# Kernel optimization log

Measured on AMD Instinct MI355X. Metric: run time of the kernel, lower is better.

## Reference

```python
import jax, jax.numpy as jnp
import numpy as np


def setup_inputs() -> dict:
    key = jax.random.key(0)
    kq, kk, kv = jax.random.split(key, 3)
    B, H, S, D = 2, 16, 2048, 64
    return {
        "query": jax.random.normal(kq, (B, H, S, D), dtype=jnp.float32),
        "key": jax.random.normal(kk, (B, H, S, D), dtype=jnp.float32),
        "value": jax.random.normal(kv, (B, H, S, D), dtype=jnp.float32),
    }


def reference(query, key, value):
    # scores = Q K^T / sqrt(d_k)   -> [B, H, S, S]
    d_k = query.shape[-1]
    scale = 1.0 / jnp.sqrt(jnp.asarray(d_k, dtype=query.dtype))
    scores = jnp.einsum("bhqd,bhkd->bhqk", query, key) * scale
    # mask=None path (the module's mask path is unreachable due to a source bug)
    p_attn = jax.nn.softmax(scores, axis=-1)
    out = jnp.einsum("bhqk,bhkd->bhqd", p_attn, value)
    return (out, p_attn)
```

## Files before the change

kernel.cpp:

```cpp
#include <hip/hip_runtime.h>
#include <hip/hip_bf16.h>
#include <cstdint>
#include <cstddef>

#define S_LEN 2048
#define D_HEAD 64
#define NBH 32
#define NELEM 4194304
#define SUP 128

typedef __attribute__((ext_vector_type(8))) short short8;
typedef __attribute__((ext_vector_type(4))) float f32x4;

__device__ __forceinline__ short f2bf(float f) {
    union { float f; uint32_t u; } v; v.f = f;
    uint32_t u = v.u + 0x7FFFu + ((v.u >> 16) & 1u);
    return (short)(u >> 16);
}

__device__ __forceinline__ uint32_t pkbf(float lo, float hi) {
    return ((uint32_t)(uint16_t)f2bf(hi) << 16) | (uint32_t)(uint16_t)f2bf(lo);
}

__global__ void convert_kf_kernel(const float* __restrict__ K, short* __restrict__ Kf) {
    const int s = blockIdx.x * 256 + threadIdx.x;
    const int l = s & 63;
    const int p = (s >> 6) & 1;
    const int g = (s >> 7) & 127;
    const int bh = s >> 14;
    const float* src = K + ((size_t)bh * S_LEN + g * 16 + (l & 15)) * D_HEAD
                         + p * 32 + (l >> 4) * 8;
    short8 y;
    #pragma unroll
    for (int e = 0; e < 8; ++e) y[e] = f2bf(src[e]);
    *reinterpret_cast<short8*>(Kf + (size_t)s * 8) = y;
}

__global__ void transpose_vf_kernel(const float* __restrict__ V, short* __restrict__ Vf) {
    __shared__ float tile[64][65];
    const int bh = blockIdx.y;
    const int s0 = blockIdx.x * 64;
    const int d = threadIdx.x & 63;
    const int r = threadIdx.x >> 6;
    const float* vp = V + ((size_t)bh * S_LEN + s0) * D_HEAD;
    #pragma unroll
    for (int i = 0; i < 16; ++i) {
        int srow = i * 4 + r;
        tile[srow][d] = vp[(size_t)srow * D_HEAD + d];
    }
    __syncthreads();
    #pragma unroll
    for (int h = 0; h < 2; ++h) {
        const int sl = h * 256 + threadIdx.x;
        const int ti = sl >> 8;
        const int vt = (sl >> 6) & 3;
        const int l  = sl & 63;
        const int lrow = l & 15, lgrp = l >> 4;
        short8 y;
        #pragma unroll
        for (int e = 0; e < 8; ++e)
            y[e] = f2bf(tile[ti * 32 + lgrp * 8 + e][vt * 16 + lrow]);
        *reinterpret_cast<short8*>(
            Vf + ((((size_t)bh * 64 + (s0 >> 5) + ti) * 4 + vt) * 64 + l) * 8) = y;
    }
}

__launch_bounds__(256, 2)
__global__ void attn_kernel(const float* __restrict__ Q,
                            const short* __restrict__ Kf,
                            const short* __restrict__ Vf,
                            float* __restrict__ Out,
                            float* __restrict__ P) {
    __shared__ __align__(16) float stage[4][2][16][SUP];

    const int lane = threadIdx.x & 63;
    const int w    = threadIdx.x >> 6;
    const int b    = blockIdx.y * 16 + blockIdx.x;
    const int swzb = (b & 7) * 64 + (b >> 3);
    const int bx   = swzb & 15;
    const int bh   = swzb >> 4;
    const int qb   = bx * 128 + w * 32;
    const int lrow = lane & 15;
    const int lgrp = lane >> 4;
    const float scale = 0.125f;

    short8 qa0A, qa1A, qa0B, qa1B;
    {
        const float* qrA = Q + ((size_t)bh * S_LEN + qb + lrow) * D_HEAD + lgrp * 8;
        const float* qrB = qrA + 16 * D_HEAD;
        #pragma unroll
        for (int e = 0; e < 8; ++e) qa0A[e] = f2bf(qrA[e]);
        #pragma unroll
        for (int e = 0; e < 8; ++e) qa1A[e] = f2bf(qrA[e + 32]);
        #pragma unroll
        for (int e = 0; e < 8; ++e) qa0B[e] = f2bf(qrB[e]);
        #pragma unroll
        for (int e = 0; e < 8; ++e) qa1B[e] = f2bf(qrB[e + 32]);
    }

    const short* Kp = Kf + (size_t)bh * (S_LEN * D_HEAD);
    const short* Vp = Vf + (size_t)bh * (S_LEN * D_HEAD);
    const int lofs = lane * 8;

    const int srcA = ((lane & 15) + ((lane >> 4) & 1) * 32) << 2;
    const int srcB = srcA + (16 << 2);
    const bool glow = (lgrp < 2);

    float lA = 0.f, lB = 0.f;
    f32x4 accA[4] = {}, accB[4] = {};
    for (int j0 = 0; j0 < S_LEN; j0 += 32) {
        const short* kg = Kp + (size_t)(j0 >> 4) * 1024;
        short8 k00 = *reinterpret_cast<const short8*>(kg + lofs);
        short8 k01 = *reinterpret_cast<const short8*>(kg + 512 + lofs);
        short8 k10 = *reinterpret_cast<const short8*>(kg + 1024 + lofs);
        short8 k11 = *reinterpret_cast<const short8*>(kg + 1536 + lofs);
        const short* vg = Vp + (size_t)(j0 >> 5) * 2048;
        short8 bv0 = *reinterpret_cast<const short8*>(vg + lofs);
        short8 bv1 = *reinterpret_cast<const short8*>(vg + 512 + lofs);
        short8 bv2 = *reinterpret_cast<const short8*>(vg + 1024 + lofs);
        short8 bv3 = *reinterpret_cast<const short8*>(vg + 1536 + lofs);

        {
            f32x4 c0 = {0.f, 0.f, 0.f, 0.f};
            f32x4 c1 = {0.f, 0.f, 0.f, 0.f};
            c0 = __builtin_amdgcn_mfma_f32_16x16x32_bf16(k00, qa0A, c0, 0, 0, 0);
            c0 = __builtin_amdgcn_mfma_f32_16x16x32_bf16(k01, qa1A, c0, 0, 0, 0);
            c1 = __builtin_amdgcn_mfma_f32_16x16x32_bf16(k10, qa0A, c1, 0, 0, 0);
            c1 = __builtin_amdgcn_mfma_f32_16x16x32_bf16(k11, qa1A, c1, 0, 0, 0);
            float e0[4], e1[4];
            #pragma unroll
            for (int rr = 0; rr < 4; ++rr) {
                e0[rr] = __expf(c0[rr] * scale);
                e1[rr] = __expf(c1[rr] * scale);
                lA += e0[rr] + e1[rr];
            }
            int w00 = (int)pkbf(e0[0], e0[1]);
            int w01 = (int)pkbf(e0[2], e0[3]);
            int w10 = (int)pkbf(e1[0], e1[1]);
            int w11 = (int)pkbf(e1[2], e1[3]);
            int t0 = __builtin_amdgcn_ds_bpermute(srcA, w00);
            int t1 = __builtin_amdgcn_ds_bpermute(srcA, w01);
            int t2 = __builtin_amdgcn_ds_bpermute(srcB, w00);
            int t3 = __builtin_amdgcn_ds_bpermute(srcB, w01);
            int u0 = __builtin_amdgcn_ds_bpermute(srcA, w10);
            int u1 = __builtin_amdgcn_ds_bpermute(srcA, w11);
            int u2 = __builtin_amdgcn_ds_bpermute(srcB, w10);
            int u3 = __builtin_amdgcn_ds_bpermute(srcB, w11);
            union { short8 s8; int wd[4]; } fr;
            fr.wd[0] = glow ? t0 : u0;
            fr.wd[1] = glow ? t1 : u1;
            fr.wd[2] = glow ? t2 : u2;
            fr.wd[3] = glow ? t3 : u3;
            accA[0] = __builtin_amdgcn_mfma_f32_16x16x32_bf16(fr.s8, bv0, accA[0], 0, 0, 0);
            accA[1] = __builtin_amdgcn_mfma_f32_16x16x32_bf16(fr.s8, bv1, accA[1], 0, 0, 0);
            accA[2] = __builtin_amdgcn_mfma_f32_16x16x32_bf16(fr.s8, bv2, accA[2], 0, 0, 0);
            accA[3] = __builtin_amdgcn_mfma_f32_16x16x32_bf16(fr.s8, bv3, accA[3], 0, 0, 0);
        }
        {
            f32x4 c0 = {0.f, 0.f, 0.f, 0.f};
            f32x4 c1 = {0.f, 0.f, 0.f, 0.f};
            c0 = __builtin_amdgcn_mfma_f32_16x16x32_bf16(k00, qa0B, c0, 0, 0, 0);
            c0 = __builtin_amdgcn_mfma_f32_16x16x32_bf16(k01, qa1B, c0, 0, 0, 0);
            c1 = __builtin_amdgcn_mfma_f32_16x16x32_bf16(k10, qa0B, c1, 0, 0, 0);
            c1 = __builtin_amdgcn_mfma_f32_16x16x32_bf16(k11, qa1B, c1, 0, 0, 0);
            float e0[4], e1[4];
            #pragma unroll
            for (int rr = 0; rr < 4; ++rr) {
                e0[rr] = __expf(c0[rr] * scale);
                e1[rr] = __expf(c1[rr] * scale);
                lB += e0[rr] + e1[rr];
            }
            int w00 = (int)pkbf(e0[0], e0[1]);
            int w01 = (int)pkbf(e0[2], e0[3]);
            int w10 = (int)pkbf(e1[0], e1[1]);
            int w11 = (int)pkbf(e1[2], e1[3]);
            int t0 = __builtin_amdgcn_ds_bpermute(srcA, w00);
            int t1 = __builtin_amdgcn_ds_bpermute(srcA, w01);
            int t2 = __builtin_amdgcn_ds_bpermute(srcB, w00);
            int t3 = __builtin_amdgcn_ds_bpermute(srcB, w01);
            int u0 = __builtin_amdgcn_ds_bpermute(srcA, w10);
            int u1 = __builtin_amdgcn_ds_bpermute(srcA, w11);
            int u2 = __builtin_amdgcn_ds_bpermute(srcB, w10);
            int u3 = __builtin_amdgcn_ds_bpermute(srcB, w11);
            union { short8 s8; int wd[4]; } fr;
            fr.wd[0] = glow ? t0 : u0;
            fr.wd[1] = glow ? t1 : u1;
            fr.wd[2] = glow ? t2 : u2;
            fr.wd[3] = glow ? t3 : u3;
            accB[0] = __builtin_amdgcn_mfma_f32_16x16x32_bf16(fr.s8, bv0, accB[0], 0, 0, 0);
            accB[1] = __builtin_amdgcn_mfma_f32_16x16x32_bf16(fr.s8, bv1, accB[1], 0, 0, 0);
            accB[2] = __builtin_amdgcn_mfma_f32_16x16x32_bf16(fr.s8, bv2, accB[2], 0, 0, 0);
            accB[3] = __builtin_amdgcn_mfma_f32_16x16x32_bf16(fr.s8, bv3, accB[3], 0, 0, 0);
        }
    }
    lA += __shfl_xor(lA, 16);  lA += __shfl_xor(lA, 32);
    lB += __shfl_xor(lB, 16);  lB += __shfl_xor(lB, 32);
    const float rlA = 1.0f / lA;
    const float rlB = 1.0f / lB;

    {
        float rloA[4], rloB[4];
        #pragma unroll
        for (int rr = 0; rr < 4; ++rr) {
            rloA[rr] = __shfl(rlA, lgrp * 4 + rr);
            rloB[rr] = __shfl(rlB, lgrp * 4 + rr);
        }
        float* obA = Out + ((size_t)bh * S_LEN + qb + lgrp * 4) * D_HEAD + lrow;
        float* obB = obA + (size_t)16 * D_HEAD;
        #pragma unroll
        for (int vt = 0; vt < 4; ++vt) {
            #pragma unroll
            for (int rr = 0; rr < 4; ++rr) {
                obA[(size_t)rr * D_HEAD + vt * 16] = accA[vt][rr] * rloA[rr];
                obB[(size_t)rr * D_HEAD + vt * 16] = accB[vt][rr] * rloB[rr];
            }
        }
    }

    char* stgA = (char*)&stage[w][0][0][0];
    char* stgB = (char*)&stage[w][1][0][0];
    const int swz = (lrow & 7) << 4;
    float* Pb = P + (size_t)bh * S_LEN * S_LEN;

    short8 pk00[4], pk01[4], pk10[4], pk11[4];
    #pragma unroll
    for (int jj = 0; jj < 4; ++jj) {
        const short* kg = Kp + (size_t)((jj * 32) >> 4) * 1024;
        pk00[jj] = *reinterpret_cast<const short8*>(kg + lofs);
        pk01[jj] = *reinterpret_cast<const short8*>(kg + 512 + lofs);
        pk10[jj] = *reinterpret_cast<const short8*>(kg + 1024 + lofs);
        pk11[jj] = *reinterpret_cast<const short8*>(kg + 1536 + lofs);
    }

    for (int sup = 0; sup < S_LEN; sup += SUP) {
        #pragma unroll
        for (int jj = 0; jj < SUP / 32; ++jj) {
            short8 k00 = pk00[jj], k01 = pk01[jj], k10 = pk10[jj], k11 = pk11[jj];
            const int o0 = (lrow * 512 + ((jj * 32 + lgrp * 4) << 2)) ^ swz;
            const int o1 = (lrow * 512 + ((jj * 32 + 16 + lgrp * 4) << 2)) ^ swz;
            {
                f32x4 c0 = {0.f, 0.f, 0.f, 0.f};
                f32x4 c1 = {0.f, 0.f, 0.f, 0.f};
                c0 = __builtin_amdgcn_mfma_f32_16x16x32_bf16(k00, qa0A, c0, 0, 0, 0);
                c0 = __builtin_amdgcn_mfma_f32_16x16x32_bf16(k01, qa1A, c0, 0, 0, 0);
                c1 = __builtin_amdgcn_mfma_f32_16x16x32_bf16(k10, qa0A, c1, 0, 0, 0);
                c1 = __builtin_amdgcn_mfma_f32_16x16x32_bf16(k11, qa1A, c1, 0, 0, 0);
                f32x4 p0, p1;
                #pragma unroll
                for (int rr = 0; rr < 4; ++rr) {
                    p0[rr] = __expf(c0[rr] * scale) * rlA;
                    p1[rr] = __expf(c1[rr] * scale) * rlA;
                }
                *(f32x4*)(stgA + o0) = p0;
                *(f32x4*)(stgA + o1) = p1;
            }
            {
                f32x4 c0 = {0.f, 0.f, 0.f, 0.f};
                f32x4 c1 = {0.f, 0.f, 0.f, 0.f};
                c0 = __builtin_amdgcn_mfma_f32_16x16x32_bf16(k00, qa0B, c0, 0, 0, 0);
                c0 = __builtin_amdgcn_mfma_f32_16x16x32_bf16(k01, qa1B, c0, 0, 0, 0);
                c1 = __builtin_amdgcn_mfma_f32_16x16x32_bf16(k10, qa0B, c1, 0, 0, 0);
                c1 = __builtin_amdgcn_mfma_f32_16x16x32_bf16(k11, qa1B, c1, 0, 0, 0);
                f32x4 p0, p1;
                #pragma unroll
                for (int rr = 0; rr < 4; ++rr) {
                    p0[rr] = __expf(c0[rr] * scale) * rlB;
                    p1[rr] = __expf(c1[rr] * scale) * rlB;
                }
                *(f32x4*)(stgB + o0) = p0;
                *(f32x4*)(stgB + o1) = p1;
            }
        }

        asm volatile("s_waitcnt lgkmcnt(0)" ::: "memory");

        {
            const int nsup = (sup + SUP < S_LEN) ? (sup + SUP) : 0;
            #pragma unroll
            for (int jj = 0; jj < 4; ++jj) {
                const short* kg = Kp + (size_t)((nsup + jj * 32) >> 4) * 1024;
                pk00[jj] = *reinterpret_cast<const short8*>(kg + lofs);
                pk01[jj] = *reinterpret_cast<const short8*>(kg + 512 + lofs);
                pk10[jj] = *reinterpret_cast<const short8*>(kg + 1024 + lofs);
                pk11[jj] = *reinterpret_cast<const short8*>(kg + 1536 + lofs);
            }
        }
        __builtin_amdgcn_sched_barrier(0);

        #pragma unroll
        for (int rb = 0; rb < 8; ++rb) {
            const int r = rb * 2 + (lane >> 5);
            const int c = lane & 31;
            f32x4 pv = *(const f32x4*)(stgA + ((r * 512 + c * 16) ^ ((r & 7) << 4)));
            __builtin_nontemporal_store(pv,
                (f32x4*)(Pb + (size_t)(qb + r) * S_LEN + sup + c * 4));
        }
        #pragma unroll
        for (int rb = 0; rb < 8; ++rb) {
            const int r = rb * 2 + (lane >> 5);
            const int c = lane & 31;
            f32x4 pv = *(const f32x4*)(stgB + ((r * 512 + c * 16) ^ ((r & 7) << 4)));
            __builtin_nontemporal_store(pv,
                (f32x4*)(Pb + (size_t)(qb + 16 + r) * S_LEN + sup + c * 4));
        }
        asm volatile("s_waitcnt lgkmcnt(0)" ::: "memory");
    }
}

extern "C" void kernel_launch(void* const* d_in, const int* in_sizes, int n_in,
                              void* d_out, int out_size, void* d_ws, size_t ws_size,
                              hipStream_t stream) {
    const float* Q = (const float*)d_in[0];
    const float* K = (const float*)d_in[1];
    const float* V = (const float*)d_in[2];
    float* Out = (float*)d_out;
    float* P = Out + (size_t)NELEM;
    short* Kf = (short*)d_ws;
    short* Vf = Kf + (size_t)NELEM;

    convert_kf_kernel<<<NELEM / (256 * 8), 256, 0, stream>>>(K, Kf);
    transpose_vf_kernel<<<dim3(S_LEN / 64, NBH), 256, 0, stream>>>(V, Vf);
    attn_kernel<<<dim3(S_LEN / 128, NBH), 256, 0, stream>>>(Q, Kf, Vf, Out, P);
}
```

Measured before the change: 175.2 us.

## Stage P tiles as bf16 in shared memory and flush every two super-blocks

The probability tile is now kept in LDS as packed bf16 instead of fp32. This halves the staging footprint, so two 128-column super-blocks fit in the same space. The global write-out now runs once per pair of super-blocks with 256-column rows per store pass, which halves the number of LDS sync/flush phases. The cost is that P values written to global memory are truncated to bf16 precision, which may break tolerance on the fp32 p_attn output.

```diff
diff --git a/kernel.cpp b/kernel.cpp
--- a/kernel.cpp
+++ b/kernel.cpp
@@ -71,7 +71,7 @@
                             const short* __restrict__ Vf,
                             float* __restrict__ Out,
                             float* __restrict__ P) {
-    __shared__ __align__(16) float stage[4][2][16][SUP];
+    __shared__ __align__(16) unsigned short stage[4][2][16][256];
 
     const int lane = threadIdx.x & 63;
     const int w    = threadIdx.x >> 6;
@@ -219,7 +219,7 @@
 
     char* stgA = (char*)&stage[w][0][0][0];
     char* stgB = (char*)&stage[w][1][0][0];
-    const int swz = (lrow & 7) << 4;
+    const int swz2 = (lrow & 7) << 4;
     float* Pb = P + (size_t)bh * S_LEN * S_LEN;
 
     short8 pk00[4], pk01[4], pk10[4], pk11[4];
@@ -233,11 +233,13 @@
     }
 
     for (int sup = 0; sup < S_LEN; sup += SUP) {
+        const int h = (sup >> 7) & 1;
         #pragma unroll
         for (int jj = 0; jj < SUP / 32; ++jj) {
             short8 k00 = pk00[jj], k01 = pk01[jj], k10 = pk10[jj], k11 = pk11[jj];
-            const int o0 = (lrow * 512 + ((jj * 32 + lgrp * 4) << 2)) ^ swz;
-            const int o1 = (lrow * 512 + ((jj * 32 + 16 + lgrp * 4) << 2)) ^ swz;
+            const int cb = h * 256 + ((jj * 32 + lgrp * 4) << 1);
+            const int o0 = lrow * 512 + (cb ^ swz2);
+            const int o1 = lrow * 512 + ((cb + 32) ^ swz2);
             {
                 f32x4 c0 = {0.f, 0.f, 0.f, 0.f};
                 f32x4 c1 = {0.f, 0.f, 0.f, 0.f};
@@ -251,8 +253,8 @@
                     p0[rr] = __expf(c0[rr] * scale) * rlA;
                     p1[rr] = __expf(c1[rr] * scale) * rlA;
                 }
-                *(f32x4*)(stgA + o0) = p0;
-                *(f32x4*)(stgA + o1) = p1;
+                *(uint2*)(stgA + o0) = make_uint2(pkbf(p0[0], p0[1]), pkbf(p0[2], p0[3]));
+                *(uint2*)(stgA + o1) = make_uint2(pkbf(p1[0], p1[1]), pkbf(p1[2], p1[3]));
             }
             {
                 f32x4 c0 = {0.f, 0.f, 0.f, 0.f};
@@ -267,12 +269,10 @@
                     p0[rr] = __expf(c0[rr] * scale) * rlB;
                     p1[rr] = __expf(c1[rr] * scale) * rlB;
                 }
-                *(f32x4*)(stgB + o0) = p0;
-                *(f32x4*)(stgB + o1) = p1;
-            }
-        }
-
-        asm volatile("s_waitcnt lgkmcnt(0)" ::: "memory");
+                *(uint2*)(stgB + o0) = make_uint2(pkbf(p0[0], p0[1]), pkbf(p0[2], p0[3]));
+                *(uint2*)(stgB + o1) = make_uint2(pkbf(p1[0], p1[1]), pkbf(p1[2], p1[3]));
+            }
+        }
 
         {
             const int nsup = (sup + SUP < S_LEN) ? (sup + SUP) : 0;
@@ -285,25 +285,33 @@
                 pk11[jj] = *reinterpret_cast<const short8*>(kg + 1536 + lofs);
             }
         }
-        __builtin_amdgcn_sched_barrier(0);
-
-        #pragma unroll
-        for (int rb = 0; rb < 8; ++rb) {
-            const int r = rb * 2 + (lane >> 5);
-            const int c = lane & 31;
-            f32x4 pv = *(const f32x4*)(stgA + ((r * 512 + c * 16) ^ ((r & 7) << 4)));
-            __builtin_nontemporal_store(pv,
-                (f32x4*)(Pb + (size_t)(qb + r) * S_LEN + sup + c * 4));
-        }
-        #pragma unroll
-        for (int rb = 0; rb < 8; ++rb) {
-            const int r = rb * 2 + (lane >> 5);
-            const int c = lane & 31;
-            f32x4 pv = *(const f32x4*)(stgB + ((r * 512 + c * 16) ^ ((r & 7) << 4)));
-            __builtin_nontemporal_store(pv,
-                (f32x4*)(Pb + (size_t)(qb + 16 + r) * S_LEN + sup + c * 4));
-        }
-        asm volatile("s_waitcnt lgkmcnt(0)" ::: "memory");
+
+        if (h == 1) {
+            asm volatile("s_waitcnt lgkmcnt(0)" ::: "memory");
+            __builtin_amdgcn_sched_barrier(0);
+            const int supW = sup - SUP;
+            #pragma unroll
+            for (int r = 0; r < 16; ++r) {
+                uint2 v = *(const uint2*)(stgA + r * 512 + ((lane * 8) ^ ((r & 7) << 4)));
+                union { float f; uint32_t u; } e0, e1, e2, e3;
+                e0.u = v.x << 16;  e1.u = v.x & 0xFFFF0000u;
+                e2.u = v.y << 16;  e3.u = v.y & 0xFFFF0000u;
+                f32x4 o = {e0.f, e1.f, e2.f, e3.f};
+                __builtin_nontemporal_store(o,
+                    (f32x4*)(Pb + (size_t)(qb + r) * S_LEN + supW + lane * 4));
+            }
+            #pragma unroll
+            for (int r = 0; r < 16; ++r) {
+                uint2 v = *(const uint2*)(stgB + r * 512 + ((lane * 8) ^ ((r & 7) << 4)));
+                union { float f; uint32_t u; } e0, e1, e2, e3;
+                e0.u = v.x << 16;  e1.u = v.x & 0xFFFF0000u;
+                e2.u = v.y << 16;  e3.u = v.y & 0xFFFF0000u;
+                f32x4 o = {e0.f, e1.f, e2.f, e3.f};
+                __builtin_nontemporal_store(o,
+                    (f32x4*)(Pb + (size_t)(qb + 16 + r) * S_LEN + supW + lane * 4));
+            }
+            asm volatile("s_waitcnt lgkmcnt(0)" ::: "memory");
+        }
     }
 }
 
```

After: 183.8 us. 1.05x slower.

## Stagger row-group passes so the PV product fuses with P write

Applied to the files above, without the earlier changes.

The two 16-row groups per wave are now processed in staggered passes. Group A computes its row sum and PV output in a first pass. A second pass writes A's normalized P while also accumulating B's row sum. A third pass writes B's P and computes B's PV from the already-normalized probabilities, so B no longer needs a separate full sweep. The intent is to remove one complete QK^T/exp sweep for half the rows by fusing the output product with the P write. In exchange the loop structure becomes more complex, shared staging shrinks to a single buffer, and B's P@V now uses normalized bf16 probabilities.

```diff
diff --git a/kernel.cpp b/kernel.cpp
--- a/kernel.cpp
+++ b/kernel.cpp
@@ -7,7 +7,6 @@
 #define D_HEAD 64
 #define NBH 32
 #define NELEM 4194304
-#define SUP 128
 
 typedef __attribute__((ext_vector_type(8))) short short8;
 typedef __attribute__((ext_vector_type(4))) float f32x4;
@@ -71,7 +70,7 @@
                             const short* __restrict__ Vf,
                             float* __restrict__ Out,
                             float* __restrict__ P) {
-    __shared__ __align__(16) float stage[4][2][16][SUP];
+    __shared__ __align__(16) float stage[4][16][128];
 
     const int lane = threadIdx.x & 63;
     const int w    = threadIdx.x >> 6;
@@ -106,8 +105,8 @@
     const int srcB = srcA + (16 << 2);
     const bool glow = (lgrp < 2);
 
-    float lA = 0.f, lB = 0.f;
-    f32x4 accA[4] = {}, accB[4] = {};
+    float lA = 0.f;
+    f32x4 accA[4] = {};
     for (int j0 = 0; j0 < S_LEN; j0 += 32) {
         const short* kg = Kp + (size_t)(j0 >> 4) * 1024;
         short8 k00 = *reinterpret_cast<const short8*>(kg + lofs);
@@ -120,24 +119,172 @@
         short8 bv2 = *reinterpret_cast<const short8*>(vg + 1024 + lofs);
         short8 bv3 = *reinterpret_cast<const short8*>(vg + 1536 + lofs);
 
+        f32x4 c0 = {0.f, 0.f, 0.f, 0.f};
+        f32x4 c1 = {0.f, 0.f, 0.f, 0.f};
+        c0 = __builtin_amdgcn_mfma_f32_16x16x32_bf16(k00, qa0A, c0, 0, 0, 0);
+        c0 = __builtin_amdgcn_mfma_f32_16x16x32_bf16(k01, qa1A, c0, 0, 0, 0);
+        c1 = __builtin_amdgcn_mfma_f32_16x16x32_bf16(k10, qa0A, c1, 0, 0, 0);
+        c1 = __builtin_amdgcn_mfma_f32_16x16x32_bf16(k11, qa1A, c1, 0, 0, 0);
+        float e0[4], e1[4];
+        #pragma unroll
+        for (int rr = 0; rr < 4; ++rr) {
+            e0[rr] = __expf(c0[rr] * scale);
+            e1[rr] = __expf(c1[rr] * scale);
+            lA += e0[rr] + e1[rr];
+        }
+        int w00 = (int)pkbf(e0[0], e0[1]);
+        int w01 = (int)pkbf(e0[2], e0[3]);
+        int w10 = (int)pkbf(e1[0], e1[1]);
+        int w11 = (int)pkbf(e1[2], e1[3]);
+        int t0 = __builtin_amdgcn_ds_bpermute(srcA, w00);
+        int t1 = __builtin_amdgcn_ds_bpermute(srcA, w01);
+        int t2 = __builtin_amdgcn_ds_bpermute(srcB, w00);
+        int t3 = __builtin_amdgcn_ds_bpermute(srcB, w01);
+        int u0 = __builtin_amdgcn_ds_bpermute(srcA, w10);
+        int u1 = __builtin_amdgcn_ds_bpermute(srcA, w11);
+        int u2 = __builtin_amdgcn_ds_bpermute(srcB, w10);
+        int u3 = __builtin_amdgcn_ds_bpermute(srcB, w11);
+        union { short8 s8; int wd[4]; } fr;
+        fr.wd[0] = glow ? t0 : u0;
+        fr.wd[1] = glow ? t1 : u1;
+        fr.wd[2] = glow ? t2 : u2;
+        fr.wd[3] = glow ? t3 : u3;
+        accA[0] = __builtin_amdgcn_mfma_f32_16x16x32_bf16(fr.s8, bv0, accA[0], 0, 0, 0);
+        accA[1] = __builtin_amdgcn_mfma_f32_16x16x32_bf16(fr.s8, bv1, accA[1], 0, 0, 0);
+        accA[2] = __builtin_amdgcn_mfma_f32_16x16x32_bf16(fr.s8, bv2, accA[2], 0, 0, 0);
+        accA[3] = __builtin_amdgcn_mfma_f32_16x16x32_bf16(fr.s8, bv3, accA[3], 0, 0, 0);
+    }
+    lA += __shfl_xor(lA, 16);  lA += __shfl_xor(lA, 32);
+    const float rlA = 1.0f / lA;
+
+    {
+        float rloA[4];
+        #pragma unroll
+        for (int rr = 0; rr < 4; ++rr) rloA[rr] = __shfl(rlA, lgrp * 4 + rr);
+        float* obA = Out + ((size_t)bh * S_LEN + qb + lgrp * 4) * D_HEAD + lrow;
+        #pragma unroll
+        for (int vt = 0; vt < 4; ++vt) {
+            #pragma unroll
+            for (int rr = 0; rr < 4; ++rr)
+                obA[(size_t)rr * D_HEAD + vt * 16] = accA[vt][rr] * rloA[rr];
+        }
+    }
+
+    char* stg = (char*)&stage[w][0][0];
+    const int swz2 = (lrow & 7) << 4;
+    float* Pb = P + (size_t)bh * S_LEN * S_LEN;
+    float lB = 0.f;
+
+    short8 pk[4][4];
+    #pragma unroll
+    for (int jj = 0; jj < 4; ++jj) {
+        const short* kg = Kp + (size_t)((jj * 32) >> 4) * 1024;
+        pk[jj][0] = *reinterpret_cast<const short8*>(kg + lofs);
+        pk[jj][1] = *reinterpret_cast<const short8*>(kg + 512 + lofs);
+        pk[jj][2] = *reinterpret_cast<const short8*>(kg + 1024 + lofs);
+        pk[jj][3] = *reinterpret_cast<const short8*>(kg + 1536 + lofs);
+    }
+
+    for (int sup = 0; sup < S_LEN; sup += 128) {
+        #pragma unroll
+        for (int jj = 0; jj < 4; ++jj) {
+            short8 k00 = pk[jj][0], k01 = pk[jj][1], k10 = pk[jj][2], k11 = pk[jj][3];
+            {
+                f32x4 d0 = {0.f, 0.f, 0.f, 0.f};
+                f32x4 d1 = {0.f, 0.f, 0.f, 0.f};
+                d0 = __builtin_amdgcn_mfma_f32_16x16x32_bf16(k00, qa0B, d0, 0, 0, 0);
+                d0 = __builtin_amdgcn_mfma_f32_16x16x32_bf16(k01, qa1B, d0, 0, 0, 0);
+                d1 = __builtin_amdgcn_mfma_f32_16x16x32_bf16(k10, qa0B, d1, 0, 0, 0);
+                d1 = __builtin_amdgcn_mfma_f32_16x16x32_bf16(k11, qa1B, d1, 0, 0, 0);
+                #pragma unroll
+                for (int rr = 0; rr < 4; ++rr)
+                    lB += __expf(d0[rr] * scale) + __expf(d1[rr] * scale);
+            }
+            {
+                f32x4 c0 = {0.f, 0.f, 0.f, 0.f};
+                f32x4 c1 = {0.f, 0.f, 0.f, 0.f};
+                c0 = __builtin_amdgcn_mfma_f32_16x16x32_bf16(k00, qa0A, c0, 0, 0, 0);
+                c0 = __builtin_amdgcn_mfma_f32_16x16x32_bf16(k01, qa1A, c0, 0, 0, 0);
+                c1 = __builtin_amdgcn_mfma_f32_16x16x32_bf16(k10, qa0A, c1, 0, 0, 0);
+                c1 = __builtin_amdgcn_mfma_f32_16x16x32_bf16(k11, qa1A, c1, 0, 0, 0);
+                f32x4 p0, p1;
+                #pragma unroll
+                for (int rr = 0; rr < 4; ++rr) {
+                    p0[rr] = __expf(c0[rr] * scale) * rlA;
+                    p1[rr] = __expf(c1[rr] * scale) * rlA;
+                }
+                const int o0 = (lrow * 512 + ((jj * 32 + lgrp * 4) << 2)) ^ swz2;
+                const int o1 = (lrow * 512 + ((jj * 32 + 16 + lgrp * 4) << 2)) ^ swz2;
+                *(f32x4*)(stg + o0) = p0;
+                *(f32x4*)(stg + o1) = p1;
+            }
+        }
+        asm volatile("s_waitcnt lgkmcnt(0)" ::: "memory");
         {
+            const int nsup = (sup + 128 < S_LEN) ? (sup + 128) : 0;
+            #pragma unroll
+            for (int jj = 0; jj < 4; ++jj) {
+                const short* kg = Kp + (size_t)((nsup + jj * 32) >> 4) * 1024;
+                pk[jj][0] = *reinterpret_cast<const short8*>(kg + lofs);
+                pk[jj][1] = *reinterpret_cast<const short8*>(kg + 512 + lofs);
+                pk[jj][2] = *reinterpret_cast<const short8*>(kg + 1024 + lofs);
+                pk[jj][3] = *reinterpret_cast<const short8*>(kg + 1536 + lofs);
+            }
+        }
+        __builtin_amdgcn_sched_barrier(0);
+        #pragma unroll
+        for (int rb = 0; rb < 8; ++rb) {
+            const int r = rb * 2 + (lane >> 5);
+            const int c = lane & 31;
+            f32x4 pv = *(const f32x4*)(stg + ((r * 512 + c * 16) ^ ((r & 7) << 4)));
+            __builtin_nontemporal_store(pv,
+                (f32x4*)(Pb + (size_t)(qb + r) * S_LEN + sup + c * 4));
+        }
+        asm volatile("s_waitcnt lgkmcnt(0)" ::: "memory");
+    }
+    lB += __shfl_xor(lB, 16);  lB += __shfl_xor(lB, 32);
+    const float rlB = 1.0f / lB;
+
+    f32x4 accB[4] = {};
+    short8 qk[2][4], qv[2][4];
+    #pragma unroll
+    for (int jj = 0; jj < 2; ++jj) {
+        const short* kg = Kp + (size_t)((jj * 32) >> 4) * 1024;
+        qk[jj][0] = *reinterpret_cast<const short8*>(kg + lofs);
+        qk[jj][1] = *reinterpret_cast<const short8*>(kg + 512 + lofs);
+        qk[jj][2] = *reinterpret_cast<const short8*>(kg + 1024 + lofs);
+        qk[jj][3] = *reinterpret_cast<const short8*>(kg + 1536 + lofs);
+        const short* vg = Vp + (size_t)((jj * 32) >> 5) * 2048;
+        qv[jj][0] = *reinterpret_cast<const short8*>(vg + lofs);
+        qv[jj][1] = *reinterpret_cast<const short8*>(vg + 512 + lofs);
+        qv[jj][2] = *reinterpret_cast<const short8*>(vg + 1024 + lofs);
+        qv[jj][3] = *reinterpret_cast<const short8*>(vg + 1536 + lofs);
+    }
+
+    for (int sup = 0; sup < S_LEN; sup += 64) {
+        #pragma unroll
+        for (int jj = 0; jj < 2; ++jj) {
+            short8 k00 = qk[jj][0], k01 = qk[jj][1], k10 = qk[jj][2], k11 = qk[jj][3];
             f32x4 c0 = {0.f, 0.f, 0.f, 0.f};
             f32x4 c1 = {0.f, 0.f, 0.f, 0.f};
-            c0 = __builtin_amdgcn_mfma_f32_16x16x32_bf16(k00, qa0A, c0, 0, 0, 0);
-            c0 = __builtin_amdgcn_mfma_f32_16x16x32_bf16(k01, qa1A, c0, 0, 0, 0);
-            c1 = __builtin_amdgcn_mfma_f32_16x16x32_bf16(k10, qa0A, c1, 0, 0, 0);
-            c1 = __builtin_amdgcn_mfma_f32_16x16x32_bf16(k11, qa1A, c1, 0, 0, 0);
-            float e0[4], e1[4];
+            c0 = __builtin_amdgcn_mfma_f32_16x16x32_bf16(k00, qa0B, c0, 0, 0, 0);
+            c0 = __builtin_amdgcn_mfma_f32_16x16x32_bf16(k01, qa1B, c0, 0, 0, 0);
+            c1 = __builtin_amdgcn_mfma_f32_16x16x32_bf16(k10, qa0B, c1, 0, 0, 0);
+            c1 = __builtin_amdgcn_mfma_f32_16x16x32_bf16(k11, qa1B, c1, 0, 0, 0);
+            f32x4 p0, p1;
             #pragma unroll
             for (int rr = 0; rr < 4; ++rr) {
-                e0[rr] = __expf(c0[rr] * scale);
-                e1[rr] = __expf(c1[rr] * scale);
-                lA += e0[rr] + e1[rr];
-            }
-            int w00 = (int)pkbf(e0[0], e0[1]);
-            int w01 = (int)pkbf(e0[2], e0[3]);
-            int w10 = (int)pkbf(e1[0], e1[1]);
-            int w11 = (int)pkbf(e1[2], e1[3]);
+                p0[rr] = __expf(c0[rr] * scale) * rlB;
+                p1[rr] = __expf(c1[rr] * scale) * rlB;
+            }
+            const int o0 = (lrow * 256 + ((jj * 32 + lgrp * 4) << 2)) ^ swz2;
+            const int o1 = (lrow * 256 + ((jj * 32 + 16 + lgrp * 4) << 2)) ^ swz2;
+            *(f32x4*)(stg + o0) = p0;
+            *(f32x4*)(stg + o1) = p1;
+            int w00 = (int)pkbf(p0[0], p0[1]);
+            int w01 = (int)pkbf(p0[2], p0[3]);
+            int w10 = (int)pkbf(p1[0], p1[1]);
+            int w11 = (int)pkbf(p1[2], p1[3]);
             int t0 = __builtin_amdgcn_ds_bpermute(srcA, w00);
             int t1 = __builtin_amdgcn_ds_bpermute(srcA, w01);
             int t2 = __builtin_amdgcn_ds_bpermute(srcB, w00);
@@ -151,159 +298,48 @@
             fr.wd[1] = glow ? t1 : u1;
             fr.wd[2] = glow ? t2 : u2;
             fr.wd[3] = glow ? t3 : u3;
-            accA[0] = __builtin_amdgcn_mfma_f32_16x16x32_bf16(fr.s8, bv0, accA[0], 0, 0, 0);
-            accA[1] = __builtin_amdgcn_mfma_f32_16x16x32_bf16(fr.s8, bv1, accA[1], 0, 0, 0);
-            accA[2] = __builtin_amdgcn_mfma_f32_16x16x32_bf16(fr.s8, bv2, accA[2], 0, 0, 0);
-            accA[3] = __builtin_amdgcn_mfma_f32_16x16x32_bf16(fr.s8, bv3, accA[3], 0, 0, 0);
-        }
+            accB[0] = __builtin_amdgcn_mfma_f32_16x16x32_bf16(fr.s8, qv[jj][0], accB[0], 0, 0, 0);
+            accB[1] = __builtin_amdgcn_mfma_f32_16x16x32_bf16(fr.s8, qv[jj][1], accB[1], 0, 0, 0);
+            accB[2] = __builtin_amdgcn_mfma_f32_16x16x32_bf16(fr.s8, qv[jj][2], accB[2], 0, 0, 0);
+            accB[3] = __builtin_amdgcn_mfma_f32_16x16x32_bf16(fr.s8, qv[jj][3], accB[3], 0, 0, 0);
+        }
+        asm volatile("s_waitcnt lgkmcnt(0)" ::: "memory");
         {
-            f32x4 c0 = {0.f, 0.f, 0.f, 0.f};
-            f32x4 c1 = {0.f, 0.f, 0.f, 0.f};
-            c0 = __builtin_amdgcn_mfma_f32_16x16x32_bf16(k00, qa0B, c0, 0, 0, 0);
-            c0 = __builtin_amdgcn_mfma_f32_16x16x32_bf16(k01, qa1B, c0, 0, 0, 0);
-            c1 = __builtin_amdgcn_mfma_f32_16x16x32_bf16(k10, qa0B, c1, 0, 0, 0);
-            c1 = __builtin_amdgcn_mfma_f32_16x16x32_bf16(k11, qa1B, c1, 0, 0, 0);
-            float e0[4], e1[4];
-            #pragma unroll
-            for (int rr = 0; rr < 4; ++rr) {
-                e0[rr] = __expf(c0[rr] * scale);
-                e1[rr] = __expf(c1[rr] * scale);
-                lB += e0[rr] + e1[rr];
-            }
-            int w00 = (int)pkbf(e0[0], e0[1]);
-            int w01 = (int)pkbf(e0[2], e0[3]);
-            int w10 = (int)pkbf(e1[0], e1[1]);
-            int w11 = (int)pkbf(e1[2], e1[3]);
-            int t0 = __builtin_amdgcn_ds_bpermute(srcA, w00);
-            int t1 = __builtin_amdgcn_ds_bpermute(srcA, w01);
-            int t2 = __builtin_amdgcn_ds_bpermute(srcB, w00);
-            int t3 = __builtin_amdgcn_ds_bpermute(srcB, w01);
-            int u0 = __builtin_amdgcn_ds_bpermute(srcA, w10);
-            int u1 = __builtin_amdgcn_ds_bpermute(srcA, w11);
-            int u2 = __builtin_amdgcn_ds_bpermute(srcB, w10);
-            int u3 = __builtin_amdgcn_ds_bpermute(srcB, w11);
-            union { short8 s8; int wd[4]; } fr;
-            fr.wd[0] = glow ? t0 : u0;
-            fr.wd[1] = glow ? t1 : u1;
-            fr.wd[2] = glow ? t2 : u2;
-            fr.wd[3] = glow ? t3 : u3;
-            accB[0] = __builtin_amdgcn_mfma_f32_16x16x32_bf16(fr.s8, bv0, accB[0], 0, 0, 0);
-            accB[1] = __builtin_amdgcn_mfma_f32_16x16x32_bf16(fr.s8, bv1, accB[1], 0, 0, 0);
-            accB[2] = __builtin_amdgcn_mfma_f32_16x16x32_bf16(fr.s8, bv2, accB[2], 0, 0, 0);
-            accB[3] = __builtin_amdgcn_mfma_f32_16x16x32_bf16(fr.s8, bv3, accB[3], 0, 0, 0);
-        }
-    }
-    lA += __shfl_xor(lA, 16);  lA += __shfl_xor(lA, 32);
-    lB += __shfl_xor(lB, 16);  lB += __shfl_xor(lB, 32);
-    const float rlA = 1.0f / lA;
-    const float rlB = 1.0f / lB;
-
-    {
-        float rloA[4], rloB[4];
-        #pragma unroll
-        for (int rr = 0; rr < 4; ++rr) {
-            rloA[rr] = __shfl(rlA, lgrp * 4 + rr);
-            rloB[rr] = __shfl(rlB, lgrp * 4 + rr);
-        }
-        float* obA = Out + ((size_t)bh * S_LEN + qb + lgrp * 4) * D_HEAD + lrow;
-        float* obB = obA + (size_t)16 * D_HEAD;
-        #pragma unroll
-        for (int vt = 0; vt < 4; ++vt) {
-            #pragma unroll
-            for (int rr = 0; rr < 4; ++rr) {
-                obA[(size_t)rr * D_HEAD + vt * 16] = accA[vt][rr] * rloA[rr];
-                obB[(size_t)rr * D_HEAD + vt * 16] = accB[vt][rr] * rloB[rr];
-            }
-        }
-    }
-
-    char* stgA = (char*)&stage[w][0][0][0];
-    char* stgB = (char*)&stage[w][1][0][0];
-    const int swz = (lrow & 7) << 4;
-    float* Pb = P + (size_t)bh * S_LEN * S_LEN;
-
-    short8 pk00[4], pk01[4], pk10[4], pk11[4];
-    #pragma unroll
-    for (int jj = 0; jj < 4; ++jj) {
-        const short* kg = Kp + (size_t)((jj * 32) >> 4) * 1024;
-        pk00[jj] = *reinterpret_cast<const short8*>(kg + lofs);
-        pk01[jj] = *reinterpret_cast<const short8*>(kg + 512 + lofs);
-        pk10[jj] = *reinterpret_cast<const short8*>(kg + 1024 + lofs);
-        pk11[jj] = *reinterpret_cast<const short8*>(kg + 1536 + lofs);
-    }
-
-    for (int sup = 0; sup < S_LEN; sup += SUP) {
-        #pragma unroll
-        for (int jj = 0; jj < SUP / 32; ++jj) {
-            short8 k00 = pk00[jj], k01 = pk01[jj], k10 = pk10[jj], k11 = pk11[jj];
-            const int o0 = (lrow * 512 + ((jj * 32 + lgrp * 4) << 2)) ^ swz;
-            const int o1 = (lrow * 512 + ((jj * 32 + 16 + lgrp * 4) << 2)) ^ swz;
-            {
-                f32x4 c0 = {0.f, 0.f, 0.f, 0.f};
-                f32x4 c1 = {0.f, 0.f, 0.f, 0.f};
-                c0 = __builtin_amdgcn_mfma_f32_16x16x32_bf16(k00, qa0A, c0, 0, 0, 0);
-                c0 = __builtin_amdgcn_mfma_f32_16x16x32_bf16(k01, qa1A, c0, 0, 0, 0);
-                c1 = __builtin_amdgcn_mfma_f32_16x16x32_bf16(k10, qa0A, c1, 0, 0, 0);
-                c1 = __builtin_amdgcn_mfma_f32_16x16x32_bf16(k11, qa1A, c1, 0, 0, 0);
-                f32x4 p0, p1;
-                #pragma unroll
-                for (int rr = 0; rr < 4; ++rr) {
-                    p0[rr] = __expf(c0[rr] * scale) * rlA;
-                    p1[rr] = __expf(c1[rr] * scale) * rlA;
-                }
-                *(f32x4*)(stgA + o0) = p0;
-                *(f32x4*)(stgA + o1) = p1;
-            }
-            {
-                f32x4 c0 = {0.f, 0.f, 0.f, 0.f};
-                f32x4 c1 = {0.f, 0.f, 0.f, 0.f};
-                c0 = __builtin_amdgcn_mfma_f32_16x16x32_bf16(k00, qa0B, c0, 0, 0, 0);
-                c0 = __builtin_amdgcn_mfma_f32_16x16x32_bf16(k01, qa1B, c0, 0, 0, 0);
-                c1 = __builtin_amdgcn_mfma_f32_16x16x32_bf16(k10, qa0B, c1, 0, 0, 0);
-                c1 = __builtin_amdgcn_mfma_f32_16x16x32_bf16(k11, qa1B, c1, 0, 0, 0);
-                f32x4 p0, p1;
-                #pragma unroll
-                for (int rr = 0; rr < 4; ++rr) {
-                    p0[rr] = __expf(c0[rr] * scale) * rlB;
-                    p1[rr] = __expf(c1[rr] * scale) * rlB;
-                }
-                *(f32x4*)(stgB + o0) = p0;
-                *(f32x4*)(stgB + o1) = p1;
-            }
-        }
-
-        asm volatile("s_waitcnt lgkmcnt(0)" ::: "memory");
-
-        {
-            const int nsup = (sup + SUP < S_LEN) ? (sup + SUP) : 0;
-            #pragma unroll
-            for (int jj = 0; jj < 4; ++jj) {
+            const int nsup = (sup + 64 < S_LEN) ? (sup + 64) : 0;
+            #pragma unroll
+            for (int jj = 0; jj < 2; ++jj) {
                 const short* kg = Kp + (size_t)((nsup + jj * 32) >> 4) * 1024;
-                pk00[jj] = *reinterpret_cast<const short8*>(kg + lofs);
-                pk01[jj] = *reinterpret_cast<const short8*>(kg + 512 + lofs);
-                pk10[jj] = *reinterpret_cast<const short8*>(kg + 1024 + lofs);
-                pk11[jj] = *reinterpret_cast<const short8*>(kg + 1536 + lofs);
+                qk[jj][0] = *reinterpret_cast<const short8*>(kg + lofs);
+                qk[jj][1] = *reinterpret_cast<const short8*>(kg + 512 + lofs);
+                qk[jj][2] = *reinterpret_cast<const short8*>(kg + 1024 + lofs);
+                qk[jj][3] = *reinterpret_cast<const short8*>(kg + 1536 + lofs);
+                const short* vg = Vp + (size_t)((nsup + jj * 32) >> 5) * 2048;
+                qv[jj][0] = *reinterpret_cast<const short8*>(vg + lofs);
+                qv[jj][1] = *reinterpret_cast<const short8*>(vg + 512 + lofs);
+                qv[jj][2] = *reinterpret_cast<const short8*>(vg + 1024 + lofs);
+                qv[jj][3] = *reinterpret_cast<const short8*>(vg + 1536 + lofs);
             }
         }
         __builtin_amdgcn_sched_barrier(0);
-
-        #pragma unroll
-        for (int rb = 0; rb < 8; ++rb) {
-            const int r = rb * 2 + (lane >> 5);
-            const int c = lane & 31;
-            f32x4 pv = *(const f32x4*)(stgA + ((r * 512 + c * 16) ^ ((r & 7) << 4)));
-            __builtin_nontemporal_store(pv,
-                (f32x4*)(Pb + (size_t)(qb + r) * S_LEN + sup + c * 4));
-        }
-        #pragma unroll
-        for (int rb = 0; rb < 8; ++rb) {
-            const int r = rb * 2 + (lane >> 5);
-            const int c = lane & 31;
-            f32x4 pv = *(const f32x4*)(stgB + ((r * 512 + c * 16) ^ ((r & 7) << 4)));
+        #pragma unroll
+        for (int rb = 0; rb < 4; ++rb) {
+            const int r = rb * 4 + (lane >> 4);
+            const int c = lane & 15;
+            f32x4 pv = *(const f32x4*)(stg + r * 256 + ((c * 16) ^ ((r & 7) << 4)));
             __builtin_nontemporal_store(pv,
                 (f32x4*)(Pb + (size_t)(qb + 16 + r) * S_LEN + sup + c * 4));
         }
         asm volatile("s_waitcnt lgkmcnt(0)" ::: "memory");
+    }
+
+    {
+        float* obB = Out + ((size_t)bh * S_LEN + qb + 16 + lgrp * 4) * D_HEAD + lrow;
+        #pragma unroll
+        for (int vt = 0; vt < 4; ++vt) {
+            #pragma unroll
+            for (int rr = 0; rr < 4; ++rr)
+                obB[(size_t)rr * D_HEAD + vt * 16] = accB[vt][rr];
+        }
     }
 }
 
```

After: 175.7 us. No clear change (+0.2%).
